# Performance work log

Hardware: AMD Instinct MI355X
Metric: run time of the kernel (lower is better)

## Reference

```python
import jax, jax.numpy as jnp
import numpy as np

N, S, E, H = 2, 2048, 1024, 16
D = E // H  # head dim = 64


def setup_inputs() -> dict:
    key = jax.random.key(0)
    ks = jax.random.split(key, 9)
    queries = jax.random.normal(ks[0], (N, S, E), dtype=jnp.float32)
    keys = jax.random.normal(ks[1], (N, S, E), dtype=jnp.float32)
    values = jax.random.normal(ks[2], (N, S, E), dtype=jnp.float32)
    mask = jax.random.randint(ks[3], (N, H, S, S), 0, 2, dtype=jnp.int32)
    # torch nn.Linear weights: shape (out_features, in_features), y = x @ W.T
    sc = 1.0 / np.sqrt(E)
    Wq = jax.random.uniform(ks[4], (E, E), jnp.float32, -sc, sc)
    Wk = jax.random.uniform(ks[5], (E, E), jnp.float32, -sc, sc)
    Wv = jax.random.uniform(ks[6], (E, E), jnp.float32, -sc, sc)
    Wo = jax.random.uniform(ks[7], (E, E), jnp.float32, -sc, sc)
    bo = jax.random.uniform(ks[8], (E,), jnp.float32, -sc, sc)
    return {"queries": queries, "keys": keys, "values": values, "mask": mask,
            "Wq": Wq, "Wk": Wk, "Wv": Wv, "Wo": Wo, "bo": bo}


def reference(queries, keys, values, mask, Wq, Wk, Wv, Wo, bo):
    n, d_q, _ = queries.shape
    d_k = keys.shape[1]
    q = (queries @ Wq.T).reshape(n, d_q, H, D)
    k = (keys @ Wk.T).reshape(n, d_k, H, D)
    v = (values @ Wv.T).reshape(n, d_k, H, D)
    energy = jnp.einsum('nqhd,nkhd->nhqk', q, k)
    energy = jnp.where(mask == 0, jnp.float32(-1e20), energy)
    # NOTE: module scales by sqrt of KEY SEQUENCE LENGTH, not head dim
    attn = jax.nn.softmax(energy / (d_k ** 0.5), axis=3)
    out = jnp.einsum('nhql,nlhd->nqhd', attn, v).reshape(n, d_q, E)
    return out @ Wo.T + bo
```

## Files before the change

kernel.cpp:

```cpp
#include <hip/hip_runtime.h>
#include <hip/hip_bf16.h>

#define DEVI __device__ __forceinline__

typedef __bf16 bf16x8 __attribute__((ext_vector_type(8)));
typedef float f32x4 __attribute__((ext_vector_type(4)));
typedef unsigned short u16x4 __attribute__((ext_vector_type(4)));
typedef unsigned int u32x2 __attribute__((ext_vector_type(2)));
typedef int i32x4 __attribute__((ext_vector_type(4)));

constexpr int Nn = 2, Ss = 2048, Ee = 1024, Hh = 16;
constexpr int Ms = Nn * Ss;
constexpr float SCALE = 0.022097086912079608f;

constexpr size_t SZ_X   = (size_t)Ms * Ee;
constexpr size_t OFF_QB = 0;
constexpr size_t OFF_KB = SZ_X;
constexpr size_t OFF_VB = 2 * SZ_X;
constexpr size_t OFF_XQ = 3 * SZ_X;
constexpr size_t OFF_W  = 6 * SZ_X;
constexpr size_t OFF_ATTN = OFF_XQ;

DEVI unsigned short f2bf(float f) {
  unsigned int u = __builtin_bit_cast(unsigned int, f);
  u += 0x7fffu + ((u >> 16) & 1u);
  return (unsigned short)(u >> 16);
}

DEVI void async16(const void* g, void* l) {
  __builtin_amdgcn_global_load_lds(
      (const __attribute__((address_space(1))) void*)g,
      (__attribute__((address_space(3))) void*)l, 16, 0, 0);
}

DEVI f32x4 mfma_bf16(bf16x8 a, bf16x8 b, f32x4 c) {
  return __builtin_amdgcn_mfma_f32_16x16x32_bf16(a, b, c, 0, 0, 0);
}

DEVI unsigned cvt_pk_bf16(float lo, float hi) {
  unsigned r;
  asm("v_cvt_pk_bf16_f32 %0, %1, %2" : "=v"(r) : "v"(lo), "v"(hi));
  return r;
}

__global__ __launch_bounds__(256) void cvt_batch(
    const float* __restrict__ s0, const float* __restrict__ s1,
    const float* __restrict__ s2, const float* __restrict__ s3,
    unsigned short* __restrict__ dbase, size_t dstride, int n4)
{
  const float* s = (blockIdx.z == 0) ? s0 : (blockIdx.z == 1) ? s1
                 : (blockIdx.z == 2) ? s2 : s3;
  unsigned short* d = dbase + (size_t)blockIdx.z * dstride;
  const int i = blockIdx.x * 256 + threadIdx.x;
  if (i >= n4) return;
  const float4 v = reinterpret_cast<const float4*>(s)[i];
  u16x4 o = { f2bf(v.x), f2bf(v.y), f2bf(v.z), f2bf(v.w) };
  reinterpret_cast<u16x4*>(d)[i] = o;
}

template <bool WRITE_F32>
__global__ __launch_bounds__(256) void gemm_bt(
    const unsigned short* __restrict__ Abase,
    const unsigned short* __restrict__ Bbase,
    unsigned short* __restrict__ Cbase,
    float* __restrict__ Cf,
    const float* __restrict__ bias,
    size_t strideA, size_t strideB, size_t strideC, int ldC)
{
  constexpr int K = 1024;
  __shared__ unsigned short As[128 * 32];
  __shared__ unsigned short Bs[128 * 32];

  const int z = blockIdx.z;
  const unsigned short* A = Abase + (size_t)z * strideA;
  const unsigned short* B = Bbase + (size_t)z * strideB;

  const int tid = threadIdx.x;
  const int lane = tid & 63, w = tid >> 6;
  const int lr = lane & 15, lg = lane >> 4;
  const int m0 = blockIdx.y * 128, n0 = blockIdx.x * 128;
  const int wr = (w >> 1) * 64, wc = (w & 1) * 64;

  const f32x4 zero = {0.f, 0.f, 0.f, 0.f};
  f32x4 acc[4][4];
  for (int a = 0; a < 4; ++a)
    for (int b = 0; b < 4; ++b) acc[a][b] = zero;

  for (int k0 = 0; k0 < K; k0 += 32) {
#pragma unroll
    for (int ii = 0; ii < 2; ++ii) {
      const int i = 2 * w + ii;
      const int boff = i * 1024 + lane * 16;
      const int row = boff >> 6;
      const int colb = boff & 63;
      const char* ga = (const char*)A + ((size_t)(m0 + row) * K + k0) * 2 + colb;
      const char* gb = (const char*)B + ((size_t)(n0 + row) * K + k0) * 2 + colb;
      async16(ga, (char*)As + i * 1024);
      async16(gb, (char*)Bs + i * 1024);
    }
    __syncthreads();

    bf16x8 aF[4], bF[4];
#pragma unroll
    for (int rb = 0; rb < 4; ++rb)
      aF[rb] = *(const bf16x8*)(As + (wr + rb * 16 + lr) * 32 + lg * 8);
#pragma unroll
    for (int cb = 0; cb < 4; ++cb)
      bF[cb] = *(const bf16x8*)(Bs + (wc + cb * 16 + lr) * 32 + lg * 8);
#pragma unroll
    for (int rb = 0; rb < 4; ++rb)
#pragma unroll
      for (int cb = 0; cb < 4; ++cb)
        acc[rb][cb] = mfma_bf16(aF[rb], bF[cb], acc[rb][cb]);
    __syncthreads();
  }

#pragma unroll
  for (int rb = 0; rb < 4; ++rb) {
#pragma unroll
    for (int cb = 0; cb < 4; ++cb) {
#pragma unroll
      for (int j = 0; j < 4; ++j) {
        const int row = m0 + wr + rb * 16 + lg * 4 + j;
        const int col = n0 + wc + cb * 16 + lr;
        const float v = acc[rb][cb][j];
        if constexpr (WRITE_F32) {
          Cf[(size_t)row * ldC + col] = v + bias[col];
        } else {
          unsigned short* C = Cbase + (size_t)z * strideC;
          C[(size_t)row * ldC + col] = f2bf(v);
        }
      }
    }
  }
}

__global__ __launch_bounds__(256) void attn_kernel(
    const unsigned short* __restrict__ Qb,
    const unsigned short* __restrict__ Kb,
    const unsigned short* __restrict__ Vtb,
    const int* __restrict__ mask,
    unsigned short* __restrict__ Ob)
{
  __shared__ unsigned short Kl0[64 * 64], Kl1[64 * 64];
  __shared__ unsigned short Vl0[64 * 64], Vl1[64 * 64];
  __shared__ unsigned short Pw[4 * 32 * 72];

  const int tid = threadIdx.x;
  const int lane = tid & 63, w = tid >> 6;
  const int lr = lane & 15, lg = lane >> 4;

  const int lid = blockIdx.x;
  const int xcd = lid & 7, slot = lid >> 3;
  const int g = xcd + 8 * (slot >> 4);
  const int n = g >> 4, h = g & 15;
  const int q0 = (slot & 15) * 128;

  bf16x8 aQ[2][2];
#pragma unroll
  for (int qb = 0; qb < 2; ++qb) {
    const unsigned short* qp =
        Qb + ((size_t)(n * Ss + q0 + w * 32 + qb * 16 + lr)) * Ee + h * 64 + lg * 8;
    aQ[qb][0] = *(const bf16x8*)(qp);
    aQ[qb][1] = *(const bf16x8*)(qp + 32);
  }

  const int sig0 = (w * 2) * 64 + lane;
  const int row0 = sig0 >> 3;
  const int c0 = (sig0 & 7) ^ (row0 & 7);
  const int row1 = row0 + 8;
  const int c1 = (sig0 & 7) ^ (row1 & 7);
  const int ldsb0 = (w * 2 + 0) * 1024;
  const int ldsb1 = (w * 2 + 1) * 1024;

  const unsigned short* kp0 = Kb + ((size_t)(n * Ss + row0) * Ee + h * 64 + c0 * 8);
  const unsigned short* kp1 = Kb + ((size_t)(n * Ss + row1) * Ee + h * 64 + c1 * 8);
  const unsigned short* vp0 = Vtb + ((size_t)(h * 64 + row0) * Ms + n * Ss + c0 * 8);
  const unsigned short* vp1 = Vtb + ((size_t)(h * 64 + row1) * Ms + n * Ss + c1 * 8);

  const int* m0p = mask + ((size_t)(n * Hh + h) * Ss + (q0 + w * 32 + lr)) * Ss
                        + lg * 4;
  const int* m1p = m0p + (size_t)16 * Ss;

  int koff[4][2];
#pragma unroll
  for (int cb = 0; cb < 4; ++cb) {
    const int row = cb * 16 + lr;
    koff[cb][0] = row * 128 + ((lg ^ (row & 7)) * 16);
    koff[cb][1] = row * 128 + (((4 + lg) ^ (row & 7)) * 16);
  }
  char* const PwW = (char*)Pw + w * (32 * 144);
  int pwo[2], pro[2];
#pragma unroll
  for (int qb = 0; qb < 2; ++qb) {
    pwo[qb] = (qb * 16 + lr) * 144 + lg * 8;
    pro[qb] = (qb * 16 + lr) * 144 + lg * 16;
  }

  const f32x4 zero = {0.f, 0.f, 0.f, 0.f};
  f32x4 oacc[2][4];
#pragma unroll
  for (int qb = 0; qb < 2; ++qb)
#pragma unroll
    for (int db = 0; db < 4; ++db) oacc[qb][db] = zero;
  float rs[2] = {0.f, 0.f};

  async16(kp0, (char*)Kl0 + ldsb0);
  async16(kp1, (char*)Kl0 + ldsb1);
  async16(vp0, (char*)Vl0 + ldsb0);
  async16(vp1, (char*)Vl0 + ldsb1);
  kp0 += (size_t)64 * Ee; kp1 += (size_t)64 * Ee; vp0 += 64; vp1 += 64;

  i32x4 mqA[2][4], mqB[2][4];
#pragma unroll
  for (int cb = 0; cb < 4; ++cb) {
    mqA[0][cb] = __builtin_nontemporal_load((const i32x4*)(m0p + cb * 16));
    mqA[1][cb] = __builtin_nontemporal_load((const i32x4*)(m1p + cb * 16));
  }

  auto tile = [&](const unsigned short* KC, const unsigned short* VC,
                  unsigned short* KN, unsigned short* VN,
                  i32x4 (&MQC)[2][4], i32x4 (&MQN)[2][4], bool pf) {
    asm volatile("s_waitcnt vmcnt(0)" ::: "memory");
    __builtin_amdgcn_s_barrier();

    if (pf) {
      async16(kp0, (char*)KN + ldsb0);
      async16(kp1, (char*)KN + ldsb1);
      async16(vp0, (char*)VN + ldsb0);
      async16(vp1, (char*)VN + ldsb1);
      kp0 += (size_t)64 * Ee; kp1 += (size_t)64 * Ee; vp0 += 64; vp1 += 64;
#pragma unroll
      for (int cb = 0; cb < 4; ++cb) {
        MQN[0][cb] = __builtin_nontemporal_load((const i32x4*)(m0p + 64 + cb * 16));
        MQN[1][cb] = __builtin_nontemporal_load((const i32x4*)(m1p + 64 + cb * 16));
      }
    }
    m0p += 64; m1p += 64;

#pragma unroll
    for (int cb = 0; cb < 4; ++cb) {
      const bf16x8 kF0 = *(const bf16x8*)((const char*)KC + koff[cb][0]);
      const bf16x8 kF1 = *(const bf16x8*)((const char*)KC + koff[cb][1]);
#pragma unroll
      for (int qb = 0; qb < 2; ++qb) {
        f32x4 a = mfma_bf16(kF0, aQ[qb][0], zero);
        a = mfma_bf16(kF1, aQ[qb][1], a);
        float p[4];
#pragma unroll
        for (int j = 0; j < 4; ++j)
          p[j] = MQC[qb][cb][j] ? __expf(a[j] * SCALE) : 0.f;
        rs[qb] += (p[0] + p[1]) + (p[2] + p[3]);
        u32x2 pd = { cvt_pk_bf16(p[0], p[1]), cvt_pk_bf16(p[2], p[3]) };
        *(u32x2*)(PwW + pwo[qb] + cb * 32) = pd;
      }
    }

    bf16x8 aP[2][2];
#pragma unroll
    for (int qb = 0; qb < 2; ++qb) {
      aP[qb][0] = *(const bf16x8*)(PwW + pro[qb]);
      aP[qb][1] = *(const bf16x8*)(PwW + pro[qb] + 64);
    }
#pragma unroll
    for (int db = 0; db < 4; ++db) {
#pragma unroll
      for (int kc = 0; kc < 2; ++kc) {
        const bf16x8 bV = *(const bf16x8*)((const char*)VC + koff[db][kc]);
#pragma unroll
        for (int qb = 0; qb < 2; ++qb)
          oacc[qb][db] = mfma_bf16(aP[qb][kc], bV, oacc[qb][db]);
      }
    }
  };

  for (int kt2 = 0; kt2 < 16; ++kt2) {
    tile(Kl0, Vl0, Kl1, Vl1, mqA, mqB, true);
    tile(Kl1, Vl1, Kl0, Vl0, mqB, mqA, kt2 != 15);
  }

  float inv[2][4];
#pragma unroll
  for (int qb = 0; qb < 2; ++qb) {
    float r = rs[qb];
    r += __shfl_xor(r, 16, 64);
    r += __shfl_xor(r, 32, 64);
#pragma unroll
    for (int j = 0; j < 4; ++j)
      inv[qb][j] = 1.0f / __shfl(r, lg * 4 + j, 64);
  }
#pragma unroll
  for (int qb = 0; qb < 2; ++qb)
#pragma unroll
    for (int db = 0; db < 4; ++db)
#pragma unroll
      for (int j = 0; j < 4; ++j) {
        const int qr = q0 + w * 32 + qb * 16 + lg * 4 + j;
        Ob[((size_t)(n * Ss + qr)) * Ee + h * 64 + db * 16 + lr] =
            f2bf(oacc[qb][db][j] * inv[qb][j]);
      }
}

extern "C" void kernel_launch(void* const* d_in, const int* in_sizes, int n_in,
                              void* d_out, int out_size, void* d_ws, size_t ws_size,
                              hipStream_t stream) {
  const float* qin = (const float*)d_in[0];
  const float* kin = (const float*)d_in[1];
  const float* vin = (const float*)d_in[2];
  const int*   msk = (const int*)d_in[3];
  const float* Wq  = (const float*)d_in[4];
  const float* Wk  = (const float*)d_in[5];
  const float* Wv  = (const float*)d_in[6];
  const float* Wo  = (const float*)d_in[7];
  const float* bo  = (const float*)d_in[8];
  unsigned short* ws = (unsigned short*)d_ws;
  const size_t EE = (size_t)Ee * Ee;

  cvt_batch<<<dim3((unsigned)(SZ_X / 4 / 256), 1, 3), 256, 0, stream>>>(
      qin, kin, vin, nullptr, ws + OFF_XQ, SZ_X, (int)(SZ_X / 4));
  cvt_batch<<<dim3((unsigned)(EE / 4 / 256), 1, 4), 256, 0, stream>>>(
      Wq, Wk, Wv, Wo, ws + OFF_W, EE, (int)(EE / 4));

  gemm_bt<false><<<dim3(8, 32, 2), 256, 0, stream>>>(
      ws + OFF_XQ, ws + OFF_W, ws + OFF_QB, nullptr, nullptr,
      SZ_X, EE, SZ_X, Ee);

  gemm_bt<false><<<dim3(32, 8, 1), 256, 0, stream>>>(
      ws + OFF_W + 2 * EE, ws + OFF_XQ + 2 * SZ_X, ws + OFF_VB, nullptr, nullptr,
      0, 0, 0, Ms);

  attn_kernel<<<dim3(512), 256, 0, stream>>>(
      ws + OFF_QB, ws + OFF_KB, ws + OFF_VB, msk, ws + OFF_ATTN);

  gemm_bt<true><<<dim3(8, 32, 1), 256, 0, stream>>>(
      ws + OFF_ATTN, ws + OFF_W + 3 * EE, nullptr,
      (float*)d_out, bo, 0, 0, 0, Ee);
}
```

Measured before the change: 247.2 us.

## Triple-buffer mask register prefetch two tiles ahead with partial vmcnt waits

Mask tiles are now loaded into a rotating set of three register buffers, issued two key tiles ahead of use instead of one. The per-tile wait drops from vmcnt(0) to vmcnt(8), so the K/V async copies can complete without waiting on the most recent mask loads. Scheduling barriers pin the load order so the counter-based wait stays valid. The cost is extra VGPRs for the third mask buffer and a loop unrolled to six tiles, which may reduce occupancy or enlarge the code.

```diff
diff --git a/kernel.cpp b/kernel.cpp
--- a/kernel.cpp
+++ b/kernel.cpp
@@ -210,32 +210,45 @@
   async16(vp0, (char*)Vl0 + ldsb0);
   async16(vp1, (char*)Vl0 + ldsb1);
   kp0 += (size_t)64 * Ee; kp1 += (size_t)64 * Ee; vp0 += 64; vp1 += 64;
-
-  i32x4 mqA[2][4], mqB[2][4];
+  __builtin_amdgcn_sched_barrier(0);
+
+  i32x4 mqA[2][4], mqB[2][4], mqC[2][4];
 #pragma unroll
   for (int cb = 0; cb < 4; ++cb) {
     mqA[0][cb] = __builtin_nontemporal_load((const i32x4*)(m0p + cb * 16));
     mqA[1][cb] = __builtin_nontemporal_load((const i32x4*)(m1p + cb * 16));
   }
+#pragma unroll
+  for (int cb = 0; cb < 4; ++cb) {
+    mqB[0][cb] = __builtin_nontemporal_load((const i32x4*)(m0p + 64 + cb * 16));
+    mqB[1][cb] = __builtin_nontemporal_load((const i32x4*)(m1p + 64 + cb * 16));
+  }
+  __builtin_amdgcn_sched_barrier(0);
 
   auto tile = [&](const unsigned short* KC, const unsigned short* VC,
                   unsigned short* KN, unsigned short* VN,
-                  i32x4 (&MQC)[2][4], i32x4 (&MQN)[2][4], bool pf) {
-    asm volatile("s_waitcnt vmcnt(0)" ::: "memory");
+                  i32x4 (&MQC)[2][4], i32x4 (&MQN)[2][4],
+                  bool do_stage, bool do_mask, bool last) {
+    if (last) asm volatile("s_waitcnt vmcnt(0)" ::: "memory");
+    else      asm volatile("s_waitcnt vmcnt(8)" ::: "memory");
     __builtin_amdgcn_s_barrier();
 
-    if (pf) {
+    if (do_stage) {
       async16(kp0, (char*)KN + ldsb0);
       async16(kp1, (char*)KN + ldsb1);
       async16(vp0, (char*)VN + ldsb0);
       async16(vp1, (char*)VN + ldsb1);
       kp0 += (size_t)64 * Ee; kp1 += (size_t)64 * Ee; vp0 += 64; vp1 += 64;
+    }
+    __builtin_amdgcn_sched_barrier(0);
+    if (do_mask) {
 #pragma unroll
       for (int cb = 0; cb < 4; ++cb) {
-        MQN[0][cb] = __builtin_nontemporal_load((const i32x4*)(m0p + 64 + cb * 16));
-        MQN[1][cb] = __builtin_nontemporal_load((const i32x4*)(m1p + 64 + cb * 16));
-      }
-    }
+        MQN[0][cb] = __builtin_nontemporal_load((const i32x4*)(m0p + 128 + cb * 16));
+        MQN[1][cb] = __builtin_nontemporal_load((const i32x4*)(m1p + 128 + cb * 16));
+      }
+    }
+    __builtin_amdgcn_sched_barrier(0);
     m0p += 64; m1p += 64;
 
 #pragma unroll
@@ -274,10 +287,16 @@
     }
   };
 
-  for (int kt2 = 0; kt2 < 16; ++kt2) {
-    tile(Kl0, Vl0, Kl1, Vl1, mqA, mqB, true);
-    tile(Kl1, Vl1, Kl0, Vl0, mqB, mqA, kt2 != 15);
-  }
+  for (int kt6 = 0; kt6 < 5; ++kt6) {
+    tile(Kl0, Vl0, Kl1, Vl1, mqA, mqC, true, true, false);
+    tile(Kl1, Vl1, Kl0, Vl0, mqB, mqA, true, true, false);
+    tile(Kl0, Vl0, Kl1, Vl1, mqC, mqB, true, true, false);
+    tile(Kl1, Vl1, Kl0, Vl0, mqA, mqC, true, true, false);
+    tile(Kl0, Vl0, Kl1, Vl1, mqB, mqA, true, true, false);
+    tile(Kl1, Vl1, Kl0, Vl0, mqC, mqB, true, true, false);
+  }
+  tile(Kl0, Vl0, Kl1, Vl1, mqA, mqC, true, false, false);
+  tile(Kl1, Vl1, Kl0, Vl0, mqB, mqA, false, false, true);
 
   float inv[2][4];
 #pragma unroll
```

New measurement: 243.5 us. No clear change (-1.5%).

## Bitpack attention mask inside fused QKV launch and read bits in attention

Applied to the files above, without the earlier changes.

Merges the Q/K and V projection GEMMs with a mask-packing pass into one launch, where extra blocks convert the int32 mask into 64-bit ballot bitmasks. The attention kernel then loads packed bits instead of int32 mask vectors, reducing its register use and memory traffic, and the output projection becomes its own kernel. The full mask is still read once, now overlapped with GEMM work, at the cost of an extra packed buffer write and a more complex tile schedule.

```diff
diff --git a/kernel.cpp b/kernel.cpp
--- a/kernel.cpp
+++ b/kernel.cpp
@@ -7,18 +7,21 @@
 typedef float f32x4 __attribute__((ext_vector_type(4)));
 typedef unsigned short u16x4 __attribute__((ext_vector_type(4)));
 typedef unsigned int u32x2 __attribute__((ext_vector_type(2)));
-typedef int i32x4 __attribute__((ext_vector_type(4)));
+typedef unsigned long long ull;
+typedef ull u64x2 __attribute__((ext_vector_type(2)));
 
 constexpr int Nn = 2, Ss = 2048, Ee = 1024, Hh = 16;
 constexpr int Ms = Nn * Ss;
 constexpr float SCALE = 0.022097086912079608f;
 
 constexpr size_t SZ_X   = (size_t)Ms * Ee;
+constexpr size_t EEc    = (size_t)Ee * Ee;
 constexpr size_t OFF_QB = 0;
 constexpr size_t OFF_KB = SZ_X;
 constexpr size_t OFF_VB = 2 * SZ_X;
 constexpr size_t OFF_XQ = 3 * SZ_X;
 constexpr size_t OFF_W  = 6 * SZ_X;
+constexpr size_t OFF_PACK = 6 * SZ_X + 4 * EEc;
 constexpr size_t OFF_ATTN = OFF_XQ;
 
 DEVI unsigned short f2bf(float f) {
@@ -58,27 +61,16 @@
   reinterpret_cast<u16x4*>(d)[i] = o;
 }
 
-template <bool WRITE_F32>
-__global__ __launch_bounds__(256) void gemm_bt(
-    const unsigned short* __restrict__ Abase,
-    const unsigned short* __restrict__ Bbase,
-    unsigned short* __restrict__ Cbase,
-    float* __restrict__ Cf,
-    const float* __restrict__ bias,
-    size_t strideA, size_t strideB, size_t strideC, int ldC)
+DEVI void gemm_core(const unsigned short* __restrict__ A,
+                    const unsigned short* __restrict__ B,
+                    unsigned short* __restrict__ C, int ldC,
+                    int m0, int n0,
+                    unsigned short* As, unsigned short* Bs)
 {
   constexpr int K = 1024;
-  __shared__ unsigned short As[128 * 32];
-  __shared__ unsigned short Bs[128 * 32];
-
-  const int z = blockIdx.z;
-  const unsigned short* A = Abase + (size_t)z * strideA;
-  const unsigned short* B = Bbase + (size_t)z * strideB;
-
   const int tid = threadIdx.x;
   const int lane = tid & 63, w = tid >> 6;
   const int lr = lane & 15, lg = lane >> 4;
-  const int m0 = blockIdx.y * 128, n0 = blockIdx.x * 128;
   const int wr = (w >> 1) * 64, wc = (w & 1) * 64;
 
   const f32x4 zero = {0.f, 0.f, 0.f, 0.f};
@@ -116,20 +108,53 @@
   }
 
 #pragma unroll
-  for (int rb = 0; rb < 4; ++rb) {
-#pragma unroll
-    for (int cb = 0; cb < 4; ++cb) {
+  for (int rb = 0; rb < 4; ++rb)
+#pragma unroll
+    for (int cb = 0; cb < 4; ++cb)
 #pragma unroll
       for (int j = 0; j < 4; ++j) {
         const int row = m0 + wr + rb * 16 + lg * 4 + j;
         const int col = n0 + wc + cb * 16 + lr;
-        const float v = acc[rb][cb][j];
-        if constexpr (WRITE_F32) {
-          Cf[(size_t)row * ldC + col] = v + bias[col];
-        } else {
-          unsigned short* C = Cbase + (size_t)z * strideC;
-          C[(size_t)row * ldC + col] = f2bf(v);
-        }
+        C[(size_t)row * ldC + col] = f2bf(acc[rb][cb][j]);
+      }
+}
+
+__global__ __launch_bounds__(256) void qkv_pack(
+    const unsigned short* __restrict__ Xq,
+    const unsigned short* __restrict__ W,
+    unsigned short* __restrict__ QKout,
+    unsigned short* __restrict__ Vtout,
+    const int* __restrict__ mask,
+    ull* __restrict__ P64)
+{
+  __shared__ unsigned short As[128 * 32];
+  __shared__ unsigned short Bs[128 * 32];
+  const int b = blockIdx.x;
+
+  if (b < 512) {
+    const int z = b >> 8, by = (b >> 3) & 31, bx = b & 7;
+    gemm_core(Xq + (size_t)z * SZ_X, W + (size_t)z * EEc,
+              QKout + (size_t)z * SZ_X, Ee, by * 128, bx * 128, As, Bs);
+  } else if (b < 768) {
+    const int v = b - 512, bx = v & 31, by = v >> 5;
+    gemm_core(W + 2 * EEc, Xq + 2 * SZ_X, Vtout, Ms, by * 128, bx * 128, As, Bs);
+  } else {
+    const int lane = threadIdx.x & 63;
+    const int gw = (b - 768) * 4 + (threadIdx.x >> 6);
+    for (int r = 0; r < 128; ++r) {
+      const size_t rgi = (size_t)r * 4096 + gw;
+      const int* mp = mask + rgi * 256 + lane;
+      const int m0 = __builtin_nontemporal_load(mp);
+      const int m1 = __builtin_nontemporal_load(mp + 64);
+      const int m2 = __builtin_nontemporal_load(mp + 128);
+      const int m3 = __builtin_nontemporal_load(mp + 192);
+      const ull b0 = __ballot(m0 != 0);
+      const ull b1 = __ballot(m1 != 0);
+      const ull b2 = __ballot(m2 != 0);
+      const ull b3 = __ballot(m3 != 0);
+      if (lane < 4) {
+        const ull v = lane == 0 ? b0 : lane == 1 ? b1 : lane == 2 ? b2 : b3;
+        P64[rgi * 4 + lane] = v;
       }
     }
   }
@@ -139,7 +164,7 @@
     const unsigned short* __restrict__ Qb,
     const unsigned short* __restrict__ Kb,
     const unsigned short* __restrict__ Vtb,
-    const int* __restrict__ mask,
+    const ull* __restrict__ P64,
     unsigned short* __restrict__ Ob)
 {
   __shared__ unsigned short Kl0[64 * 64], Kl1[64 * 64];
@@ -178,9 +203,8 @@
   const unsigned short* vp0 = Vtb + ((size_t)(h * 64 + row0) * Ms + n * Ss + c0 * 8);
   const unsigned short* vp1 = Vtb + ((size_t)(h * 64 + row1) * Ms + n * Ss + c1 * 8);
 
-  const int* m0p = mask + ((size_t)(n * Hh + h) * Ss + (q0 + w * 32 + lr)) * Ss
-                        + lg * 4;
-  const int* m1p = m0p + (size_t)16 * Ss;
+  const ull* bmr0 = P64 + ((size_t)(n * Hh + h) * Ss + q0 + w * 32 + lr) * 32;
+  const ull* bmr1 = bmr0 + 16 * 32;
 
   int koff[4][2];
 #pragma unroll
@@ -211,32 +235,27 @@
   async16(vp1, (char*)Vl0 + ldsb1);
   kp0 += (size_t)64 * Ee; kp1 += (size_t)64 * Ee; vp0 += 64; vp1 += 64;
 
-  i32x4 mqA[2][4], mqB[2][4];
-#pragma unroll
-  for (int cb = 0; cb < 4; ++cb) {
-    mqA[0][cb] = __builtin_nontemporal_load((const i32x4*)(m0p + cb * 16));
-    mqA[1][cb] = __builtin_nontemporal_load((const i32x4*)(m1p + cb * 16));
-  }
+  u64x2 bmA[2], bmB[2];
+  bmA[0] = *(const u64x2*)(bmr0);      bmA[1] = *(const u64x2*)(bmr1);
+  bmB[0] = *(const u64x2*)(bmr0 + 2);  bmB[1] = *(const u64x2*)(bmr1 + 2);
 
   auto tile = [&](const unsigned short* KC, const unsigned short* VC,
                   unsigned short* KN, unsigned short* VN,
-                  i32x4 (&MQC)[2][4], i32x4 (&MQN)[2][4], bool pf) {
+                  const u64x2* BM, int tp, u64x2* BMN, int tn, bool do_stage) {
     asm volatile("s_waitcnt vmcnt(0)" ::: "memory");
     __builtin_amdgcn_s_barrier();
 
-    if (pf) {
+    if (do_stage) {
       async16(kp0, (char*)KN + ldsb0);
       async16(kp1, (char*)KN + ldsb1);
       async16(vp0, (char*)VN + ldsb0);
       async16(vp1, (char*)VN + ldsb1);
       kp0 += (size_t)64 * Ee; kp1 += (size_t)64 * Ee; vp0 += 64; vp1 += 64;
-#pragma unroll
-      for (int cb = 0; cb < 4; ++cb) {
-        MQN[0][cb] = __builtin_nontemporal_load((const i32x4*)(m0p + 64 + cb * 16));
-        MQN[1][cb] = __builtin_nontemporal_load((const i32x4*)(m1p + 64 + cb * 16));
-      }
-    }
-    m0p += 64; m1p += 64;
+    }
+    if (BMN) {
+      BMN[0] = *(const u64x2*)(bmr0 + tn);
+      BMN[1] = *(const u64x2*)(bmr1 + tn);
+    }
 
 #pragma unroll
     for (int cb = 0; cb < 4; ++cb) {
@@ -246,10 +265,12 @@
       for (int qb = 0; qb < 2; ++qb) {
         f32x4 a = mfma_bf16(kF0, aQ[qb][0], zero);
         a = mfma_bf16(kF1, aQ[qb][1], a);
+        const unsigned nib =
+            (unsigned)(BM[qb][tp] >> (cb * 16 + lg * 4)) & 0xFu;
         float p[4];
 #pragma unroll
         for (int j = 0; j < 4; ++j)
-          p[j] = MQC[qb][cb][j] ? __expf(a[j] * SCALE) : 0.f;
+          p[j] = (nib & (1u << j)) ? __expf(a[j] * SCALE) : 0.f;
         rs[qb] += (p[0] + p[1]) + (p[2] + p[3]);
         u32x2 pd = { cvt_pk_bf16(p[0], p[1]), cvt_pk_bf16(p[2], p[3]) };
         *(u32x2*)(PwW + pwo[qb] + cb * 32) = pd;
@@ -274,9 +295,13 @@
     }
   };
 
-  for (int kt2 = 0; kt2 < 16; ++kt2) {
-    tile(Kl0, Vl0, Kl1, Vl1, mqA, mqB, true);
-    tile(Kl1, Vl1, Kl0, Vl0, mqB, mqA, kt2 != 15);
+  for (int t4 = 0; t4 < 8; ++t4) {
+    const int t = t4 * 4;
+    tile(Kl0, Vl0, Kl1, Vl1, bmA, 0, bmB, t + 2, true);
+    tile(Kl1, Vl1, Kl0, Vl0, bmA, 1, nullptr, 0, true);
+    tile(Kl0, Vl0, Kl1, Vl1, bmB, 0,
+         (t4 != 7) ? bmA : nullptr, t + 4, true);
+    tile(Kl1, Vl1, Kl0, Vl0, bmB, 1, nullptr, 0, t4 != 7);
   }
 
   float inv[2][4];
@@ -298,6 +323,66 @@
         const int qr = q0 + w * 32 + qb * 16 + lg * 4 + j;
         Ob[((size_t)(n * Ss + qr)) * Ee + h * 64 + db * 16 + lr] =
             f2bf(oacc[qb][db][j] * inv[qb][j]);
+      }
+}
+
+__global__ __launch_bounds__(256) void out_proj(
+    const unsigned short* __restrict__ A,
+    const unsigned short* __restrict__ B,
+    float* __restrict__ Cf, const float* __restrict__ bias)
+{
+  __shared__ unsigned short As[128 * 32];
+  __shared__ unsigned short Bs[128 * 32];
+  constexpr int K = 1024;
+  const int tid = threadIdx.x;
+  const int lane = tid & 63, w = tid >> 6;
+  const int lr = lane & 15, lg = lane >> 4;
+  const int m0 = blockIdx.y * 128, n0 = blockIdx.x * 128;
+  const int wr = (w >> 1) * 64, wc = (w & 1) * 64;
+
+  const f32x4 zero = {0.f, 0.f, 0.f, 0.f};
+  f32x4 acc[4][4];
+  for (int a = 0; a < 4; ++a)
+    for (int b = 0; b < 4; ++b) acc[a][b] = zero;
+
+  for (int k0 = 0; k0 < K; k0 += 32) {
+#pragma unroll
+    for (int ii = 0; ii < 2; ++ii) {
+      const int i = 2 * w + ii;
+      const int boff = i * 1024 + lane * 16;
+      const int row = boff >> 6;
+      const int colb = boff & 63;
+      const char* ga = (const char*)A + ((size_t)(m0 + row) * K + k0) * 2 + colb;
+      const char* gb = (const char*)B + ((size_t)(n0 + row) * K + k0) * 2 + colb;
+      async16(ga, (char*)As + i * 1024);
+      async16(gb, (char*)Bs + i * 1024);
+    }
+    __syncthreads();
+
+    bf16x8 aF[4], bF[4];
+#pragma unroll
+    for (int rb = 0; rb < 4; ++rb)
+      aF[rb] = *(const bf16x8*)(As + (wr + rb * 16 + lr) * 32 + lg * 8);
+#pragma unroll
+    for (int cb = 0; cb < 4; ++cb)
+      bF[cb] = *(const bf16x8*)(Bs + (wc + cb * 16 + lr) * 32 + lg * 8);
+#pragma unroll
+    for (int rb = 0; rb < 4; ++rb)
+#pragma unroll
+      for (int cb = 0; cb < 4; ++cb)
+        acc[rb][cb] = mfma_bf16(aF[rb], bF[cb], acc[rb][cb]);
+    __syncthreads();
+  }
+
+#pragma unroll
+  for (int rb = 0; rb < 4; ++rb)
+#pragma unroll
+    for (int cb = 0; cb < 4; ++cb)
+#pragma unroll
+      for (int j = 0; j < 4; ++j) {
+        const int row = m0 + wr + rb * 16 + lg * 4 + j;
+        const int col = n0 + wc + cb * 16 + lr;
+        Cf[(size_t)row * Ee + col] = acc[rb][cb][j] + bias[col];
       }
 }
 
@@ -314,25 +399,19 @@
   const float* Wo  = (const float*)d_in[7];
   const float* bo  = (const float*)d_in[8];
   unsigned short* ws = (unsigned short*)d_ws;
-  const size_t EE = (size_t)Ee * Ee;
+  ull* P64 = (ull*)(ws + OFF_PACK);
 
   cvt_batch<<<dim3((unsigned)(SZ_X / 4 / 256), 1, 3), 256, 0, stream>>>(
       qin, kin, vin, nullptr, ws + OFF_XQ, SZ_X, (int)(SZ_X / 4));
-  cvt_batch<<<dim3((unsigned)(EE / 4 / 256), 1, 4), 256, 0, stream>>>(
-      Wq, Wk, Wv, Wo, ws + OFF_W, EE, (int)(EE / 4));
-
-  gemm_bt<false><<<dim3(8, 32, 2), 256, 0, stream>>>(
-      ws + OFF_XQ, ws + OFF_W, ws + OFF_QB, nullptr, nullptr,
-      SZ_X, EE, SZ_X, Ee);
-
-  gemm_bt<false><<<dim3(32, 8, 1), 256, 0, stream>>>(
-      ws + OFF_W + 2 * EE, ws + OFF_XQ + 2 * SZ_X, ws + OFF_VB, nullptr, nullptr,
-      0, 0, 0, Ms);
+  cvt_batch<<<dim3((unsigned)(EEc / 4 / 256), 1, 4), 256, 0, stream>>>(
+      Wq, Wk, Wv, Wo, ws + OFF_W, EEc, (int)(EEc / 4));
+
+  qkv_pack<<<dim3(1792), 256, 0, stream>>>(
+      ws + OFF_XQ, ws + OFF_W, ws + OFF_QB, ws + OFF_VB, msk, P64);
 
   attn_kernel<<<dim3(512), 256, 0, stream>>>(
-      ws + OFF_QB, ws + OFF_KB, ws + OFF_VB, msk, ws + OFF_ATTN);
-
-  gemm_bt<true><<<dim3(8, 32, 1), 256, 0, stream>>>(
-      ws + OFF_ATTN, ws + OFF_W + 3 * EE, nullptr,
-      (float*)d_out, bo, 0, 0, 0, Ee);
-}
+      ws + OFF_QB, ws + OFF_KB, ws + OFF_VB, P64, ws + OFF_ATTN);
+
+  out_proj<<<dim3(8, 32), 256, 0, stream>>>(
+      ws + OFF_ATTN, ws + OFF_W + 3 * EEc, (float*)d_out, bo);
+}
```

Result: slower. 310.4 us (+25.6%).

## Coalesce attention mask loads and pack them into LDS bitmasks via ballot

Applied to the files above, without the earlier changes.

Each wave now loads the int32 mask row-contiguously, with 16 lanes covering 64 consecutive keys of one query row, instead of the old scattered 64-byte segments. The loaded values are compressed with wave ballots into 4-bit nibbles stored in a small per-wave LDS buffer, and read back in the layout the MFMA output expects. This targets the mask stream, which is the largest global memory traffic in the attention kernel, and removes the double-buffered mask registers. In exchange it adds ballot instructions, LDS writes and reads per tile, and prefetches only one tile ahead.

```diff
diff --git a/kernel.cpp b/kernel.cpp
--- a/kernel.cpp
+++ b/kernel.cpp
@@ -7,6 +7,7 @@
 typedef float f32x4 __attribute__((ext_vector_type(4)));
 typedef unsigned short u16x4 __attribute__((ext_vector_type(4)));
 typedef unsigned int u32x2 __attribute__((ext_vector_type(2)));
+typedef unsigned long long ull;
 typedef int i32x4 __attribute__((ext_vector_type(4)));
 
 constexpr int Nn = 2, Ss = 2048, Ee = 1024, Hh = 16;
@@ -14,6 +15,7 @@
 constexpr float SCALE = 0.022097086912079608f;
 
 constexpr size_t SZ_X   = (size_t)Ms * Ee;
+constexpr size_t EEc    = (size_t)Ee * Ee;
 constexpr size_t OFF_QB = 0;
 constexpr size_t OFF_KB = SZ_X;
 constexpr size_t OFF_VB = 2 * SZ_X;
@@ -145,6 +147,7 @@
   __shared__ unsigned short Kl0[64 * 64], Kl1[64 * 64];
   __shared__ unsigned short Vl0[64 * 64], Vl1[64 * 64];
   __shared__ unsigned short Pw[4 * 32 * 72];
+  __shared__ unsigned char Mb[4][32][16];
 
   const int tid = threadIdx.x;
   const int lane = tid & 63, w = tid >> 6;
@@ -178,9 +181,8 @@
   const unsigned short* vp0 = Vtb + ((size_t)(h * 64 + row0) * Ms + n * Ss + c0 * 8);
   const unsigned short* vp1 = Vtb + ((size_t)(h * 64 + row1) * Ms + n * Ss + c1 * 8);
 
-  const int* m0p = mask + ((size_t)(n * Hh + h) * Ss + (q0 + w * 32 + lr)) * Ss
-                        + lg * 4;
-  const int* m1p = m0p + (size_t)16 * Ss;
+  const int* mpw = mask + ((size_t)(n * Hh + h) * Ss + (q0 + w * 32 + lg)) * Ss
+                        + lr * 4;
 
   int koff[4][2];
 #pragma unroll
@@ -204,23 +206,24 @@
 #pragma unroll
     for (int db = 0; db < 4; ++db) oacc[qb][db] = zero;
   float rs[2] = {0.f, 0.f};
+
+  i32x4 pm[8];
+  auto mload = [&]() {
+#pragma unroll
+    for (int i = 0; i < 8; ++i)
+      pm[i] = __builtin_nontemporal_load((const i32x4*)(mpw + (size_t)(4 * i) * Ss));
+    mpw += 64;
+  };
 
   async16(kp0, (char*)Kl0 + ldsb0);
   async16(kp1, (char*)Kl0 + ldsb1);
   async16(vp0, (char*)Vl0 + ldsb0);
   async16(vp1, (char*)Vl0 + ldsb1);
   kp0 += (size_t)64 * Ee; kp1 += (size_t)64 * Ee; vp0 += 64; vp1 += 64;
-
-  i32x4 mqA[2][4], mqB[2][4];
-#pragma unroll
-  for (int cb = 0; cb < 4; ++cb) {
-    mqA[0][cb] = __builtin_nontemporal_load((const i32x4*)(m0p + cb * 16));
-    mqA[1][cb] = __builtin_nontemporal_load((const i32x4*)(m1p + cb * 16));
-  }
+  mload();
 
   auto tile = [&](const unsigned short* KC, const unsigned short* VC,
-                  unsigned short* KN, unsigned short* VN,
-                  i32x4 (&MQC)[2][4], i32x4 (&MQN)[2][4], bool pf) {
+                  unsigned short* KN, unsigned short* VN, bool pf) {
     asm volatile("s_waitcnt vmcnt(0)" ::: "memory");
     __builtin_amdgcn_s_barrier();
 
@@ -230,13 +233,21 @@
       async16(vp0, (char*)VN + ldsb0);
       async16(vp1, (char*)VN + ldsb1);
       kp0 += (size_t)64 * Ee; kp1 += (size_t)64 * Ee; vp0 += 64; vp1 += 64;
-#pragma unroll
-      for (int cb = 0; cb < 4; ++cb) {
-        MQN[0][cb] = __builtin_nontemporal_load((const i32x4*)(m0p + 64 + cb * 16));
-        MQN[1][cb] = __builtin_nontemporal_load((const i32x4*)(m1p + 64 + cb * 16));
-      }
-    }
-    m0p += 64; m1p += 64;
+    }
+
+#pragma unroll
+    for (int i = 0; i < 8; ++i) {
+      const ull b0 = __ballot(pm[i][0] != 0);
+      const ull b1 = __ballot(pm[i][1] != 0);
+      const ull b2 = __ballot(pm[i][2] != 0);
+      const ull b3 = __ballot(pm[i][3] != 0);
+      const unsigned nib = (unsigned)((b0 >> lane) & 1)
+                         | ((unsigned)((b1 >> lane) & 1) << 1)
+                         | ((unsigned)((b2 >> lane) & 1) << 2)
+                         | ((unsigned)((b3 >> lane) & 1) << 3);
+      Mb[w][4 * i + lg][lr] = (unsigned char)nib;
+    }
+    if (pf) mload();
 
 #pragma unroll
     for (int cb = 0; cb < 4; ++cb) {
@@ -246,10 +257,11 @@
       for (int qb = 0; qb < 2; ++qb) {
         f32x4 a = mfma_bf16(kF0, aQ[qb][0], zero);
         a = mfma_bf16(kF1, aQ[qb][1], a);
+        const unsigned nib = Mb[w][qb * 16 + lr][cb * 4 + lg];
         float p[4];
 #pragma unroll
         for (int j = 0; j < 4; ++j)
-          p[j] = MQC[qb][cb][j] ? __expf(a[j] * SCALE) : 0.f;
+          p[j] = ((nib >> j) & 1) ? __expf(a[j] * SCALE) : 0.f;
         rs[qb] += (p[0] + p[1]) + (p[2] + p[3]);
         u32x2 pd = { cvt_pk_bf16(p[0], p[1]), cvt_pk_bf16(p[2], p[3]) };
         *(u32x2*)(PwW + pwo[qb] + cb * 32) = pd;
@@ -275,8 +287,8 @@
   };
 
   for (int kt2 = 0; kt2 < 16; ++kt2) {
-    tile(Kl0, Vl0, Kl1, Vl1, mqA, mqB, true);
-    tile(Kl1, Vl1, Kl0, Vl0, mqB, mqA, kt2 != 15);
+    tile(Kl0, Vl0, Kl1, Vl1, true);
+    tile(Kl1, Vl1, Kl0, Vl0, kt2 != 15);
   }
 
   float inv[2][4];
@@ -314,25 +326,24 @@
   const float* Wo  = (const float*)d_in[7];
   const float* bo  = (const float*)d_in[8];
   unsigned short* ws = (unsigned short*)d_ws;
-  const size_t EE = (size_t)Ee * Ee;
 
   cvt_batch<<<dim3((unsigned)(SZ_X / 4 / 256), 1, 3), 256, 0, stream>>>(
       qin, kin, vin, nullptr, ws + OFF_XQ, SZ_X, (int)(SZ_X / 4));
-  cvt_batch<<<dim3((unsigned)(EE / 4 / 256), 1, 4), 256, 0, stream>>>(
-      Wq, Wk, Wv, Wo, ws + OFF_W, EE, (int)(EE / 4));
+  cvt_batch<<<dim3((unsigned)(EEc / 4 / 256), 1, 4), 256, 0, stream>>>(
+      Wq, Wk, Wv, Wo, ws + OFF_W, EEc, (int)(EEc / 4));
 
   gemm_bt<false><<<dim3(8, 32, 2), 256, 0, stream>>>(
       ws + OFF_XQ, ws + OFF_W, ws + OFF_QB, nullptr, nullptr,
-      SZ_X, EE, SZ_X, Ee);
+      SZ_X, EEc, SZ_X, Ee);
 
   gemm_bt<false><<<dim3(32, 8, 1), 256, 0, stream>>>(
-      ws + OFF_W + 2 * EE, ws + OFF_XQ + 2 * SZ_X, ws + OFF_VB, nullptr, nullptr,
+      ws + OFF_W + 2 * EEc, ws + OFF_XQ + 2 * SZ_X, ws + OFF_VB, nullptr, nullptr,
       0, 0, 0, Ms);
 
   attn_kernel<<<dim3(512), 256, 0, stream>>>(
       ws + OFF_QB, ws + OFF_KB, ws + OFF_VB, msk, ws + OFF_ATTN);
 
   gemm_bt<true><<<dim3(8, 32, 1), 256, 0, stream>>>(
-      ws + OFF_ATTN, ws + OFF_W + 3 * EE, nullptr,
+      ws + OFF_ATTN, ws + OFF_W + 3 * EEc, nullptr,
       (float*)d_out, bo, 0, 0, 0, Ee);
 }
```

Result: faster. 228.6 us (-7.5%).
